# Optimization experiments

Measured on AMD Instinct MI355X. Metric: run time of the kernel, lower is better.

Reference implementation:

```python
import jax, jax.numpy as jnp
import numpy as np

NEG_SLOPE = 0.05

def leaky(x):
    return jnp.where(x >= 0, x, NEG_SLOPE * x)

def segment_softmax(e, seg, num_segments):
    m = jax.ops.segment_max(e, seg, num_segments=num_segments)
    ex = jnp.exp(e - m[seg])
    s = jax.ops.segment_sum(ex, seg, num_segments=num_segments)
    return ex / s[seg]

def scatter_mean(vals, seg, num_segments):
    tot = jax.ops.segment_sum(vals, seg, num_segments=num_segments)
    cnt = jax.ops.segment_sum(jnp.ones((vals.shape[0],), vals.dtype), seg, num_segments=num_segments)
    return tot / jnp.maximum(cnt, 1.0)[:, None]

def setup_inputs() -> dict:
    key = jax.random.key(0)
    ks = jax.random.split(key, 7)
    N, E, Fn, Fe, D = 50000, 800000, 128, 64, 64
    return {
        "x": jax.random.normal(ks[0], (N, Fn), jnp.float32),
        "edge_attr": jax.random.normal(ks[1], (E, Fe), jnp.float32),
        "edge_index": jax.random.randint(ks[2], (2, E), 0, N, jnp.int64),
        "W_node": jax.random.normal(ks[3], (D, Fn), jnp.float32) * 0.05,
        "W_edge": jax.random.normal(ks[4], (D, Fe), jnp.float32) * 0.05,
        "a_node": jax.random.normal(ks[5], (2 * D,), jnp.float32) * 0.05,
        "a_edge": jax.random.normal(ks[6], (2 * D,), jnp.float32) * 0.05,
    }

def reference(x, edge_attr, edge_index, W_node, W_edge, a_node, a_edge):
    N = x.shape[0]
    E = edge_index.shape[1]
    D = W_node.shape[0]
    h = x @ W_node.T           # [N, D]
    g = edge_attr @ W_edge.T   # [E, D]

    # ----- node->node branch (with self loops) -----
    loops = jnp.arange(N, dtype=edge_index.dtype)
    i_idx = jnp.concatenate([edge_index[0], loops])  # targets [E+N]
    j_idx = jnp.concatenate([edge_index[1], loops])  # sources [E+N]
    # attention score a^T [h_i || h_j] split into halves (no concat materialized)
    hi = h @ a_node[:D]   # [N]
    hj = h @ a_node[D:]   # [N]
    e_n = leaky(hi[i_idx] + hj[j_idx])               # [E+N]
    alpha_n = segment_softmax(e_n, i_idx, N)
    x_from_nodes = scatter_mean(alpha_n[:, None] * h[j_idx], i_idx, N)  # [N, D]

    # ----- edge->node branch (each edge attends from both endpoints) -----
    i_idx_e = jnp.concatenate([edge_index[0], edge_index[1]])           # [2E]
    g2 = jnp.concatenate([g, g], axis=0)                                # g[k_idx_e], [2E, D]
    he = h @ a_edge[:D]   # [N]
    ge = g @ a_edge[D:]   # [E]
    ge2 = jnp.concatenate([ge, ge])
    e_e = leaky(he[i_idx_e] + ge2)                                      # [2E]
    alpha_e = segment_softmax(e_e, i_idx_e, N)
    x_from_edges = scatter_mean(alpha_e[:, None] * g2, i_idx_e, N)      # [N, D]

    return jnp.concatenate([leaky(x_from_nodes), leaky(x_from_edges)], axis=-1)  # [N, 2D]
```

## Files before the change

kernel.cpp:

```cpp
#include <hip/hip_runtime.h>
#include <math.h>

#define NEG_SLOPE 0.05f

__device__ __forceinline__ float leaky(float x){ return x >= 0.f ? x : NEG_SLOPE * x; }

__device__ __forceinline__ unsigned short f2bf(float f){
    unsigned u = __float_as_uint(f);
    unsigned r = u + 0x7FFFu + ((u >> 16) & 1u);
    return (unsigned short)(r >> 16);
}
__device__ __forceinline__ float bf2f(unsigned short us){
    return __uint_as_float((unsigned)us << 16);
}

__global__ __launch_bounds__(256) void k_init(int* deg_n, int* deg_o, int* ctr, int N){
    int t = blockIdx.x * blockDim.x + threadIdx.x;
    if (t == 0){ ctr[0] = 0; ctr[1] = 0; }
    int stride = gridDim.x * blockDim.x;
    for (int i = t; i < N; i += stride){ deg_n[i] = 0; deg_o[i] = 0; }
}

template<int K, bool LEAKY, bool BF16OUT>
__global__ __launch_bounds__(256) void k_gemm64(const float* __restrict__ A, const float* __restrict__ B,
                                                float* __restrict__ C, unsigned short* __restrict__ Cb,
                                                int M, int ldC){
    __shared__ float As[K][68];
    __shared__ float Bs[K][68];
    const int m0 = blockIdx.x * 64;
    const int t = threadIdx.x;
    for (int i = t; i < 16 * K; i += 256){
        int d = i & 63, kq = i >> 6;
        float4 b = *(const float4*)&B[(size_t)d * K + kq * 4];
        Bs[kq*4+0][d] = b.x; Bs[kq*4+1][d] = b.y; Bs[kq*4+2][d] = b.z; Bs[kq*4+3][d] = b.w;
    }
    for (int i = t; i < 16 * K; i += 256){
        int r = i & 63, kq = i >> 6;
        int m = m0 + r;
        float4 a = make_float4(0.f, 0.f, 0.f, 0.f);
        if (m < M) a = *(const float4*)&A[(size_t)m * K + kq * 4];
        As[kq*4+0][r] = a.x; As[kq*4+1][r] = a.y; As[kq*4+2][r] = a.z; As[kq*4+3][r] = a.w;
    }
    __syncthreads();
    const int tx = t & 15, ty = t >> 4;
    float acc[4][4] = {};
    #pragma unroll 4
    for (int k = 0; k < K; k++){
        float4 a4 = *(const float4*)&As[k][ty * 4];
        float4 b4 = *(const float4*)&Bs[k][tx * 4];
        float av[4] = {a4.x, a4.y, a4.z, a4.w};
        float bv[4] = {b4.x, b4.y, b4.z, b4.w};
        #pragma unroll
        for (int r = 0; r < 4; r++)
            #pragma unroll
            for (int c = 0; c < 4; c++)
                acc[r][c] = fmaf(av[r], bv[c], acc[r][c]);
    }
    #pragma unroll
    for (int r = 0; r < 4; r++){
        int m = m0 + ty * 4 + r;
        if (m < M){
            float4 o;
            o.x = LEAKY ? leaky(acc[r][0]) : acc[r][0];
            o.y = LEAKY ? leaky(acc[r][1]) : acc[r][1];
            o.z = LEAKY ? leaky(acc[r][2]) : acc[r][2];
            o.w = LEAKY ? leaky(acc[r][3]) : acc[r][3];
            *(float4*)&C[(size_t)m * ldC + tx * 4] = o;
            if (BF16OUT){
                uint2 u;
                u.x = (unsigned)f2bf(o.x) | ((unsigned)f2bf(o.y) << 16);
                u.y = (unsigned)f2bf(o.z) | ((unsigned)f2bf(o.w) << 16);
                *(uint2*)&Cb[(size_t)m * 64 + tx * 4] = u;
            }
        }
    }
}

__global__ __launch_bounds__(256) void k_scal(const float* __restrict__ h,
        const float* __restrict__ a_node, const float* __restrict__ a_edge,
        float* __restrict__ hi, float* __restrict__ hj, float* __restrict__ he, int N){
    int i = blockIdx.x * 256 + threadIdx.x;
    if (i >= N) return;
    const float4* hr = (const float4*)(h + (size_t)i * 64);
    const float4* a1 = (const float4*)a_node;
    const float4* a2 = (const float4*)(a_node + 64);
    const float4* a3 = (const float4*)a_edge;
    float s1 = 0.f, s2 = 0.f, s3 = 0.f;
    #pragma unroll
    for (int q = 0; q < 16; q++){
        float4 v = hr[q], w1 = a1[q], w2 = a2[q], w3 = a3[q];
        s1 += v.x*w1.x + v.y*w1.y + v.z*w1.z + v.w*w1.w;
        s2 += v.x*w2.x + v.y*w2.y + v.z*w2.z + v.w*w2.w;
        s3 += v.x*w3.x + v.y*w3.y + v.z*w3.z + v.w*w3.w;
    }
    hi[i] = s1; hj[i] = s2; he[i] = s3;
}

__global__ __launch_bounds__(256) void k_ge(const float* __restrict__ ea,
        const float* __restrict__ We, const float* __restrict__ a_edge,
        float* __restrict__ ge, unsigned short* __restrict__ eab, int E){
    __shared__ float v[64];
    if (threadIdx.x < 64){
        float s = 0.f;
        for (int d = 0; d < 64; d++) s = fmaf(We[d * 64 + threadIdx.x], a_edge[64 + d], s);
        v[threadIdx.x] = s;
    }
    __syncthreads();
    int k = blockIdx.x * 256 + threadIdx.x;
    if (k >= E) return;
    const float4* row = (const float4*)(ea + (size_t)k * 64);
    uint2* brow = (uint2*)(eab + (size_t)k * 64);
    float s = 0.f;
    #pragma unroll
    for (int q = 0; q < 16; q++){
        float4 r = row[q];
        s = fmaf(r.x, v[4*q+0], s);
        s = fmaf(r.y, v[4*q+1], s);
        s = fmaf(r.z, v[4*q+2], s);
        s = fmaf(r.w, v[4*q+3], s);
        uint2 u;
        u.x = (unsigned)f2bf(r.x) | ((unsigned)f2bf(r.y) << 16);
        u.y = (unsigned)f2bf(r.z) | ((unsigned)f2bf(r.w) << 16);
        brow[q] = u;
    }
    ge[k] = s;
}

__global__ __launch_bounds__(256) void k_count(const int* __restrict__ idx,
        int* __restrict__ deg_n, int* __restrict__ deg_o, int E, int N){
    int g = blockIdx.x & 7;
    int lo = (int)(((long long)g * N) >> 3), hi = (int)(((long long)(g + 1) * N) >> 3);
    int nblk = gridDim.x >> 3;
    int start = ((blockIdx.x >> 3) * 256) + threadIdx.x;
    int stride = nblk * 256;
    for (int k = start; k < E; k += stride){
        int i0 = idx[k], i1 = idx[E + k];
        if (i0 >= lo && i0 < hi) atomicAdd(&deg_n[i0], 1);
        if (i1 >= lo && i1 < hi) atomicAdd(&deg_o[i1], 1);
    }
}

__global__ __launch_bounds__(256) void k_off(const int* __restrict__ deg_n, const int* __restrict__ deg_o,
        int* __restrict__ deg_e,
        int* __restrict__ off_n, int* __restrict__ cur_n,
        int* __restrict__ off_e, int* __restrict__ cur_e,
        int* __restrict__ ctr, int N){
    int i = blockIdx.x * 256 + threadIdx.x;
    int lane = threadIdx.x & 63;
    int dn = 0, de = 0;
    if (i < N){
        dn = deg_n[i];
        de = dn + deg_o[i];
    }
    int pn = dn, pe = de;
    #pragma unroll
    for (int d = 1; d < 64; d <<= 1){
        int on = __shfl_up(pn, d), oe = __shfl_up(pe, d);
        if (lane >= d){ pn += on; pe += oe; }
    }
    int base_n = 0, base_e = 0;
    if (lane == 63){
        base_n = atomicAdd(&ctr[0], pn);
        base_e = atomicAdd(&ctr[1], pe);
    }
    base_n = __shfl(base_n, 63);
    base_e = __shfl(base_e, 63);
    if (i < N){
        int on = base_n + pn - dn;
        int oe = base_e + pe - de;
        off_n[i] = on; cur_n[i] = on;
        off_e[i] = oe; cur_e[i] = oe;
        deg_e[i] = de;
    }
}

__global__ __launch_bounds__(256) void k_fill(const int* __restrict__ idx,
        const float* __restrict__ hj, const float* __restrict__ ge,
        int* __restrict__ cur_n, int* __restrict__ cur_e,
        int2* __restrict__ adj_n, int2* __restrict__ adj_e, int E, int N){
    int g = blockIdx.x & 7;
    int lo = (int)(((long long)g * N) >> 3), hi = (int)(((long long)(g + 1) * N) >> 3);
    int nblk = gridDim.x >> 3;
    int start = ((blockIdx.x >> 3) * 256) + threadIdx.x;
    int stride = nblk * 256;
    for (int k = start; k < E; k += stride){
        int i0 = idx[k], i1 = idx[E + k];
        bool t0 = (i0 >= lo && i0 < hi), t1 = (i1 >= lo && i1 < hi);
        if (t0 | t1){
            int gb = __float_as_int(ge[k]);
            if (t0){
                adj_n[atomicAdd(&cur_n[i0], 1)] = make_int2(i1, __float_as_int(hj[i1]));
                adj_e[atomicAdd(&cur_e[i0], 1)] = make_int2(k, gb);
            }
            if (t1) adj_e[atomicAdd(&cur_e[i1], 1)] = make_int2(k, gb);
        }
    }
}

__global__ __launch_bounds__(256) void k_out_n(const float* __restrict__ h,
        const unsigned short* __restrict__ hb,
        const float* __restrict__ hi, const float* __restrict__ hj,
        const int* __restrict__ off_n, const int* __restrict__ deg_n,
        const int2* __restrict__ adj_n,
        float* __restrict__ out, int N){
    int lane = threadIdx.x & 63;
    int i = (blockIdx.x * 256 + threadIdx.x) >> 6;
    if (i >= N) return;
    float hi_i = hi[i];
    float wself = __expf(leaky(hi_i + hj[i]));
    float s = wself;
    float acc = wself * h[(size_t)i * 64 + lane];
    int cnt = deg_n[i];
    int p = off_n[i], e = p + cnt;
    for (; p + 4 <= e; p += 4){
        int2 r0 = adj_n[p], r1 = adj_n[p+1], r2 = adj_n[p+2], r3 = adj_n[p+3];
        float v0 = bf2f(hb[(size_t)r0.x * 64 + lane]);
        float v1 = bf2f(hb[(size_t)r1.x * 64 + lane]);
        float v2 = bf2f(hb[(size_t)r2.x * 64 + lane]);
        float v3 = bf2f(hb[(size_t)r3.x * 64 + lane]);
        float w0 = __expf(leaky(hi_i + __int_as_float(r0.y)));
        float w1 = __expf(leaky(hi_i + __int_as_float(r1.y)));
        float w2 = __expf(leaky(hi_i + __int_as_float(r2.y)));
        float w3 = __expf(leaky(hi_i + __int_as_float(r3.y)));
        acc = fmaf(w0, v0, acc); acc = fmaf(w1, v1, acc);
        acc = fmaf(w2, v2, acc); acc = fmaf(w3, v3, acc);
        s += (w0 + w1) + (w2 + w3);
    }
    for (; p < e; p++){
        int2 r = adj_n[p];
        float v = bf2f(hb[(size_t)r.x * 64 + lane]);
        float w = __expf(leaky(hi_i + __int_as_float(r.y)));
        acc = fmaf(w, v, acc); s += w;
    }
    out[(size_t)i * 128 + lane] = leaky(acc / s / (float)(cnt + 1));
}

__global__ __launch_bounds__(256) void k_out_e(const unsigned short* __restrict__ eab,
        const float* __restrict__ he,
        const int* __restrict__ off_e, const int* __restrict__ deg_e,
        const int2* __restrict__ adj_e,
        float* __restrict__ acc_ea, int N){
    int lane = threadIdx.x & 63;
    int i = (blockIdx.x * 256 + threadIdx.x) >> 6;
    if (i >= N) return;
    float he_i = he[i];
    float s = 0.f, acc = 0.f;
    int cnt = deg_e[i];
    int p = off_e[i], e = p + cnt;
    for (; p + 4 <= e; p += 4){
        int2 r0 = adj_e[p], r1 = adj_e[p+1], r2 = adj_e[p+2], r3 = adj_e[p+3];
        float v0 = bf2f(eab[(size_t)r0.x * 64 + lane]);
        float v1 = bf2f(eab[(size_t)r1.x * 64 + lane]);
        float v2 = bf2f(eab[(size_t)r2.x * 64 + lane]);
        float v3 = bf2f(eab[(size_t)r3.x * 64 + lane]);
        float w0 = __expf(leaky(he_i + __int_as_float(r0.y)));
        float w1 = __expf(leaky(he_i + __int_as_float(r1.y)));
        float w2 = __expf(leaky(he_i + __int_as_float(r2.y)));
        float w3 = __expf(leaky(he_i + __int_as_float(r3.y)));
        acc = fmaf(w0, v0, acc); acc = fmaf(w1, v1, acc);
        acc = fmaf(w2, v2, acc); acc = fmaf(w3, v3, acc);
        s += (w0 + w1) + (w2 + w3);
    }
    for (; p < e; p++){
        int2 r = adj_e[p];
        float v = bf2f(eab[(size_t)r.x * 64 + lane]);
        float w = __expf(leaky(he_i + __int_as_float(r.y)));
        acc = fmaf(w, v, acc); s += w;
    }
    float val = (cnt > 0) ? (acc / s / (float)cnt) : 0.f;
    acc_ea[(size_t)i * 64 + lane] = val;
}

extern "C" void kernel_launch(void* const* d_in, const int* in_sizes, int n_in,
                              void* d_out, int out_size, void* d_ws, size_t ws_size,
                              hipStream_t stream){
    const float* x      = (const float*)d_in[0];
    const float* ea     = (const float*)d_in[1];
    const int*   idx    = (const int*)  d_in[2];
    const float* Wn     = (const float*)d_in[3];
    const float* We     = (const float*)d_in[4];
    const float* a_node = (const float*)d_in[5];
    const float* a_edge = (const float*)d_in[6];
    float* out = (float*)d_out;

    const int N = in_sizes[0] / 128;
    const int E = in_sizes[1] / 64;

    float* p = (float*)d_ws;
    float* h      = p; p += (size_t)N * 64;
    float* hi     = p; p += N;
    float* hj     = p; p += N;
    float* he     = p; p += N;
    float* ge     = p; p += E;
    float* acc_ea = p; p += (size_t)N * 64;
    unsigned short* hb  = (unsigned short*)p; p += (size_t)N * 32;
    unsigned short* eab = (unsigned short*)p; p += (size_t)E * 32;
    int* deg_n = (int*)p; p += N;
    int* deg_o = (int*)p; p += N;
    int* deg_e = (int*)p; p += N;
    int* off_n = (int*)p; p += N;
    int* off_e = (int*)p; p += N;
    int* cur_n = (int*)p; p += N;
    int* cur_e = (int*)p; p += N;
    int* ctr   = (int*)p; p += 2;
    int2* adj_n = (int2*)p; p += (size_t)2 * E;
    int2* adj_e = (int2*)p; p += (size_t)4 * E;

    k_init<<<256, 256, 0, stream>>>(deg_n, deg_o, ctr, N);
    k_gemm64<128, false, true><<<(N + 63) / 64, 256, 0, stream>>>(x, Wn, h, hb, N, 64);
    k_scal<<<(N + 255) / 256, 256, 0, stream>>>(h, a_node, a_edge, hi, hj, he, N);
    k_ge<<<(E + 255) / 256, 256, 0, stream>>>(ea, We, a_edge, ge, eab, E);
    k_count<<<1024, 256, 0, stream>>>(idx, deg_n, deg_o, E, N);
    k_off<<<(N + 255) / 256, 256, 0, stream>>>(deg_n, deg_o, deg_e, off_n, cur_n, off_e, cur_e, ctr, N);
    k_fill<<<1024, 256, 0, stream>>>(idx, hj, ge, cur_n, cur_e, adj_n, adj_e, E, N);
    k_out_n<<<(N + 3) / 4, 256, 0, stream>>>(h, hb, hi, hj, off_n, deg_n, adj_n, out, N);
    k_out_e<<<(N + 3) / 4, 256, 0, stream>>>(eab, he, off_e, deg_e, adj_e, acc_ea, N);
    k_gemm64<64, true, false><<<(N + 63) / 64, 256, 0, stream>>>(acc_ea, We, out + 64, nullptr, N, 128);
}
```

Baseline: 698.8 us.

## Fuse projection, degree counting and edge aggregation stages into fewer kernels

Folds the attention-scalar dot products into the node GEMM epilogue using wave shuffles. It merges the edge-attribute scoring and bf16 conversion with degree counting in a new row-coalesced k_ge2. The two aggregation kernels become one launch that splits blocks between the node and edge branches. The edge branch applies the W_edge projection in shared memory, so the acc_ea buffer and the final GEMM disappear. This cuts launches and global round trips of intermediates, but degree atomics are no longer partitioned by node range, which may hurt atomic locality.

```diff
diff --git a/kernel.cpp b/kernel.cpp
--- a/kernel.cpp
+++ b/kernel.cpp
@@ -14,17 +14,24 @@
     return __uint_as_float((unsigned)us << 16);
 }
 
-__global__ __launch_bounds__(256) void k_init(int* deg_n, int* deg_o, int* ctr, int N){
+__global__ __launch_bounds__(256) void k_init(int* deg_n, int* deg_o, int* ctr,
+        float* __restrict__ vv, const float* __restrict__ We, const float* __restrict__ a_edge, int N){
     int t = blockIdx.x * blockDim.x + threadIdx.x;
     if (t == 0){ ctr[0] = 0; ctr[1] = 0; }
+    if (t < 64){
+        float s = 0.f;
+        for (int d = 0; d < 64; d++) s = fmaf(We[d * 64 + t], a_edge[64 + d], s);
+        vv[t] = s;
+    }
     int stride = gridDim.x * blockDim.x;
     for (int i = t; i < N; i += stride){ deg_n[i] = 0; deg_o[i] = 0; }
 }
 
-template<int K, bool LEAKY, bool BF16OUT>
-__global__ __launch_bounds__(256) void k_gemm64(const float* __restrict__ A, const float* __restrict__ B,
-                                                float* __restrict__ C, unsigned short* __restrict__ Cb,
-                                                int M, int ldC){
+__global__ __launch_bounds__(256) void k_gemm_h(const float* __restrict__ A, const float* __restrict__ B,
+        const float* __restrict__ a_node, const float* __restrict__ a_edge,
+        float* __restrict__ C, unsigned short* __restrict__ Cb,
+        float* __restrict__ hi, float* __restrict__ hj, float* __restrict__ he, int M){
+    const int K = 128;
     __shared__ float As[K][68];
     __shared__ float Bs[K][68];
     const int m0 = blockIdx.x * 64;
@@ -60,83 +67,68 @@
     for (int r = 0; r < 4; r++){
         int m = m0 + ty * 4 + r;
         if (m < M){
-            float4 o;
-            o.x = LEAKY ? leaky(acc[r][0]) : acc[r][0];
-            o.y = LEAKY ? leaky(acc[r][1]) : acc[r][1];
-            o.z = LEAKY ? leaky(acc[r][2]) : acc[r][2];
-            o.w = LEAKY ? leaky(acc[r][3]) : acc[r][3];
-            *(float4*)&C[(size_t)m * ldC + tx * 4] = o;
-            if (BF16OUT){
-                uint2 u;
-                u.x = (unsigned)f2bf(o.x) | ((unsigned)f2bf(o.y) << 16);
-                u.y = (unsigned)f2bf(o.z) | ((unsigned)f2bf(o.w) << 16);
-                *(uint2*)&Cb[(size_t)m * 64 + tx * 4] = u;
-            }
-        }
-    }
-}
-
-__global__ __launch_bounds__(256) void k_scal(const float* __restrict__ h,
-        const float* __restrict__ a_node, const float* __restrict__ a_edge,
-        float* __restrict__ hi, float* __restrict__ hj, float* __restrict__ he, int N){
-    int i = blockIdx.x * 256 + threadIdx.x;
-    if (i >= N) return;
-    const float4* hr = (const float4*)(h + (size_t)i * 64);
-    const float4* a1 = (const float4*)a_node;
-    const float4* a2 = (const float4*)(a_node + 64);
-    const float4* a3 = (const float4*)a_edge;
-    float s1 = 0.f, s2 = 0.f, s3 = 0.f;
+            float4 o = make_float4(acc[r][0], acc[r][1], acc[r][2], acc[r][3]);
+            *(float4*)&C[(size_t)m * 64 + tx * 4] = o;
+            uint2 u;
+            u.x = (unsigned)f2bf(o.x) | ((unsigned)f2bf(o.y) << 16);
+            u.y = (unsigned)f2bf(o.z) | ((unsigned)f2bf(o.w) << 16);
+            *(uint2*)&Cb[(size_t)m * 64 + tx * 4] = u;
+        }
+    }
+    float4 an1 = *(const float4*)&a_node[tx * 4];
+    float4 an2 = *(const float4*)&a_node[64 + tx * 4];
+    float4 ae1 = *(const float4*)&a_edge[tx * 4];
+    float p1[4], p2[4], p3[4];
     #pragma unroll
-    for (int q = 0; q < 16; q++){
-        float4 v = hr[q], w1 = a1[q], w2 = a2[q], w3 = a3[q];
-        s1 += v.x*w1.x + v.y*w1.y + v.z*w1.z + v.w*w1.w;
-        s2 += v.x*w2.x + v.y*w2.y + v.z*w2.z + v.w*w2.w;
-        s3 += v.x*w3.x + v.y*w3.y + v.z*w3.z + v.w*w3.w;
-    }
-    hi[i] = s1; hj[i] = s2; he[i] = s3;
-}
-
-__global__ __launch_bounds__(256) void k_ge(const float* __restrict__ ea,
-        const float* __restrict__ We, const float* __restrict__ a_edge,
-        float* __restrict__ ge, unsigned short* __restrict__ eab, int E){
-    __shared__ float v[64];
-    if (threadIdx.x < 64){
-        float s = 0.f;
-        for (int d = 0; d < 64; d++) s = fmaf(We[d * 64 + threadIdx.x], a_edge[64 + d], s);
-        v[threadIdx.x] = s;
-    }
-    __syncthreads();
-    int k = blockIdx.x * 256 + threadIdx.x;
-    if (k >= E) return;
-    const float4* row = (const float4*)(ea + (size_t)k * 64);
-    uint2* brow = (uint2*)(eab + (size_t)k * 64);
-    float s = 0.f;
+    for (int r = 0; r < 4; r++){
+        p1[r] = acc[r][0]*an1.x + acc[r][1]*an1.y + acc[r][2]*an1.z + acc[r][3]*an1.w;
+        p2[r] = acc[r][0]*an2.x + acc[r][1]*an2.y + acc[r][2]*an2.z + acc[r][3]*an2.w;
+        p3[r] = acc[r][0]*ae1.x + acc[r][1]*ae1.y + acc[r][2]*ae1.z + acc[r][3]*ae1.w;
+    }
     #pragma unroll
-    for (int q = 0; q < 16; q++){
-        float4 r = row[q];
-        s = fmaf(r.x, v[4*q+0], s);
-        s = fmaf(r.y, v[4*q+1], s);
-        s = fmaf(r.z, v[4*q+2], s);
-        s = fmaf(r.w, v[4*q+3], s);
-        uint2 u;
-        u.x = (unsigned)f2bf(r.x) | ((unsigned)f2bf(r.y) << 16);
-        u.y = (unsigned)f2bf(r.z) | ((unsigned)f2bf(r.w) << 16);
-        brow[q] = u;
-    }
-    ge[k] = s;
-}
-
-__global__ __launch_bounds__(256) void k_count(const int* __restrict__ idx,
-        int* __restrict__ deg_n, int* __restrict__ deg_o, int E, int N){
-    int g = blockIdx.x & 7;
-    int lo = (int)(((long long)g * N) >> 3), hi = (int)(((long long)(g + 1) * N) >> 3);
-    int nblk = gridDim.x >> 3;
-    int start = ((blockIdx.x >> 3) * 256) + threadIdx.x;
-    int stride = nblk * 256;
-    for (int k = start; k < E; k += stride){
-        int i0 = idx[k], i1 = idx[E + k];
-        if (i0 >= lo && i0 < hi) atomicAdd(&deg_n[i0], 1);
-        if (i1 >= lo && i1 < hi) atomicAdd(&deg_o[i1], 1);
+    for (int m = 1; m < 16; m <<= 1){
+        #pragma unroll
+        for (int r = 0; r < 4; r++){
+            p1[r] += __shfl_xor(p1[r], m);
+            p2[r] += __shfl_xor(p2[r], m);
+            p3[r] += __shfl_xor(p3[r], m);
+        }
+    }
+    if (tx == 0){
+        #pragma unroll
+        for (int r = 0; r < 4; r++){
+            int m = m0 + ty * 4 + r;
+            if (m < M){ hi[m] = p1[r]; hj[m] = p2[r]; he[m] = p3[r]; }
+        }
+    }
+}
+
+__global__ __launch_bounds__(256) void k_ge2(const float* __restrict__ ea, const int* __restrict__ idx,
+        const float* __restrict__ vv, float* __restrict__ ge, unsigned short* __restrict__ eab,
+        int* __restrict__ deg_n, int* __restrict__ deg_o, int E){
+    int l = threadIdx.x & 63;
+    int gw = (blockIdx.x * 256 + threadIdx.x) >> 6;
+    int nw = (gridDim.x * 256) >> 6;
+    int seg = l & 15, rl = l >> 4;
+    float4 v4 = *(const float4*)&vv[seg * 4];
+    for (int r0 = gw * 4; r0 < E; r0 += nw * 4){
+        int row = r0 + rl;
+        if (row < E){
+            float4 a = *(const float4*)&ea[(size_t)row * 64 + seg * 4];
+            float s = a.x*v4.x + a.y*v4.y + a.z*v4.z + a.w*v4.w;
+            uint2 u;
+            u.x = (unsigned)f2bf(a.x) | ((unsigned)f2bf(a.y) << 16);
+            u.y = (unsigned)f2bf(a.z) | ((unsigned)f2bf(a.w) << 16);
+            *(uint2*)&eab[(size_t)row * 64 + seg * 4] = u;
+            #pragma unroll
+            for (int m = 1; m < 16; m <<= 1) s += __shfl_xor(s, m);
+            if (seg == 0){
+                ge[row] = s;
+                int i0 = idx[row], i1 = idx[E + row];
+                atomicAdd(&deg_n[i0], 1);
+                atomicAdd(&deg_o[i1], 1);
+            }
+        }
     }
 }
 
@@ -197,78 +189,100 @@
     }
 }
 
-__global__ __launch_bounds__(256) void k_out_n(const float* __restrict__ h,
-        const unsigned short* __restrict__ hb,
-        const float* __restrict__ hi, const float* __restrict__ hj,
-        const int* __restrict__ off_n, const int* __restrict__ deg_n,
-        const int2* __restrict__ adj_n,
-        float* __restrict__ out, int N){
+__global__ __launch_bounds__(256) void k_out(const float* __restrict__ h,
+        const unsigned short* __restrict__ hb, const unsigned short* __restrict__ eab,
+        const float* __restrict__ hi, const float* __restrict__ hj, const float* __restrict__ he,
+        const float* __restrict__ We,
+        const int* __restrict__ off_n, const int* __restrict__ deg_n, const int2* __restrict__ adj_n,
+        const int* __restrict__ off_e, const int* __restrict__ deg_e, const int2* __restrict__ adj_e,
+        float* __restrict__ out, int N, int nb_node){
+    __shared__ float WeT[64][65];
+    __shared__ float valS[4][64];
     int lane = threadIdx.x & 63;
-    int i = (blockIdx.x * 256 + threadIdx.x) >> 6;
-    if (i >= N) return;
-    float hi_i = hi[i];
-    float wself = __expf(leaky(hi_i + hj[i]));
-    float s = wself;
-    float acc = wself * h[(size_t)i * 64 + lane];
-    int cnt = deg_n[i];
-    int p = off_n[i], e = p + cnt;
-    for (; p + 4 <= e; p += 4){
-        int2 r0 = adj_n[p], r1 = adj_n[p+1], r2 = adj_n[p+2], r3 = adj_n[p+3];
-        float v0 = bf2f(hb[(size_t)r0.x * 64 + lane]);
-        float v1 = bf2f(hb[(size_t)r1.x * 64 + lane]);
-        float v2 = bf2f(hb[(size_t)r2.x * 64 + lane]);
-        float v3 = bf2f(hb[(size_t)r3.x * 64 + lane]);
-        float w0 = __expf(leaky(hi_i + __int_as_float(r0.y)));
-        float w1 = __expf(leaky(hi_i + __int_as_float(r1.y)));
-        float w2 = __expf(leaky(hi_i + __int_as_float(r2.y)));
-        float w3 = __expf(leaky(hi_i + __int_as_float(r3.y)));
-        acc = fmaf(w0, v0, acc); acc = fmaf(w1, v1, acc);
-        acc = fmaf(w2, v2, acc); acc = fmaf(w3, v3, acc);
-        s += (w0 + w1) + (w2 + w3);
-    }
-    for (; p < e; p++){
-        int2 r = adj_n[p];
-        float v = bf2f(hb[(size_t)r.x * 64 + lane]);
-        float w = __expf(leaky(hi_i + __int_as_float(r.y)));
-        acc = fmaf(w, v, acc); s += w;
-    }
-    out[(size_t)i * 128 + lane] = leaky(acc / s / (float)(cnt + 1));
-}
-
-__global__ __launch_bounds__(256) void k_out_e(const unsigned short* __restrict__ eab,
-        const float* __restrict__ he,
-        const int* __restrict__ off_e, const int* __restrict__ deg_e,
-        const int2* __restrict__ adj_e,
-        float* __restrict__ acc_ea, int N){
-    int lane = threadIdx.x & 63;
-    int i = (blockIdx.x * 256 + threadIdx.x) >> 6;
-    if (i >= N) return;
-    float he_i = he[i];
-    float s = 0.f, acc = 0.f;
-    int cnt = deg_e[i];
-    int p = off_e[i], e = p + cnt;
-    for (; p + 4 <= e; p += 4){
-        int2 r0 = adj_e[p], r1 = adj_e[p+1], r2 = adj_e[p+2], r3 = adj_e[p+3];
-        float v0 = bf2f(eab[(size_t)r0.x * 64 + lane]);
-        float v1 = bf2f(eab[(size_t)r1.x * 64 + lane]);
-        float v2 = bf2f(eab[(size_t)r2.x * 64 + lane]);
-        float v3 = bf2f(eab[(size_t)r3.x * 64 + lane]);
-        float w0 = __expf(leaky(he_i + __int_as_float(r0.y)));
-        float w1 = __expf(leaky(he_i + __int_as_float(r1.y)));
-        float w2 = __expf(leaky(he_i + __int_as_float(r2.y)));
-        float w3 = __expf(leaky(he_i + __int_as_float(r3.y)));
-        acc = fmaf(w0, v0, acc); acc = fmaf(w1, v1, acc);
-        acc = fmaf(w2, v2, acc); acc = fmaf(w3, v3, acc);
-        s += (w0 + w1) + (w2 + w3);
-    }
-    for (; p < e; p++){
-        int2 r = adj_e[p];
-        float v = bf2f(eab[(size_t)r.x * 64 + lane]);
-        float w = __expf(leaky(he_i + __int_as_float(r.y)));
-        acc = fmaf(w, v, acc); s += w;
-    }
-    float val = (cnt > 0) ? (acc / s / (float)cnt) : 0.f;
-    acc_ea[(size_t)i * 64 + lane] = val;
+    int w = threadIdx.x >> 6;
+
+    if (blockIdx.x < nb_node){
+        int i = (blockIdx.x * 256 + (int)threadIdx.x) >> 6;
+        if (i >= N) return;
+        float hi_i = hi[i];
+        float wself = __expf(leaky(hi_i + hj[i]));
+        float s = wself;
+        float acc = wself * h[(size_t)i * 64 + lane];
+        int cnt = deg_n[i];
+        int p = off_n[i], e = p + cnt;
+        for (; p + 4 <= e; p += 4){
+            int2 r0 = adj_n[p], r1 = adj_n[p+1], r2 = adj_n[p+2], r3 = adj_n[p+3];
+            float v0 = bf2f(hb[(size_t)r0.x * 64 + lane]);
+            float v1 = bf2f(hb[(size_t)r1.x * 64 + lane]);
+            float v2 = bf2f(hb[(size_t)r2.x * 64 + lane]);
+            float v3 = bf2f(hb[(size_t)r3.x * 64 + lane]);
+            float w0 = __expf(leaky(hi_i + __int_as_float(r0.y)));
+            float w1 = __expf(leaky(hi_i + __int_as_float(r1.y)));
+            float w2 = __expf(leaky(hi_i + __int_as_float(r2.y)));
+            float w3 = __expf(leaky(hi_i + __int_as_float(r3.y)));
+            acc = fmaf(w0, v0, acc); acc = fmaf(w1, v1, acc);
+            acc = fmaf(w2, v2, acc); acc = fmaf(w3, v3, acc);
+            s += (w0 + w1) + (w2 + w3);
+        }
+        for (; p < e; p++){
+            int2 r = adj_n[p];
+            float v = bf2f(hb[(size_t)r.x * 64 + lane]);
+            float wgt = __expf(leaky(hi_i + __int_as_float(r.y)));
+            acc = fmaf(wgt, v, acc); s += wgt;
+        }
+        out[(size_t)i * 128 + lane] = leaky(acc / s / (float)(cnt + 1));
+    } else {
+        for (int t2 = threadIdx.x; t2 < 1024; t2 += 256){
+            int d = t2 >> 4, c0 = (t2 & 15) * 4;
+            float4 v = *(const float4*)&We[d * 64 + c0];
+            WeT[c0+0][d] = v.x; WeT[c0+1][d] = v.y; WeT[c0+2][d] = v.z; WeT[c0+3][d] = v.w;
+        }
+        int i = ((blockIdx.x - nb_node) * 256 + (int)threadIdx.x) >> 6;
+        float val = 0.f;
+        int iok = (i < N);
+        if (iok){
+            float he_i = he[i];
+            float s = 0.f, acc = 0.f;
+            int cnt = deg_e[i];
+            int p = off_e[i], e = p + cnt;
+            for (; p + 4 <= e; p += 4){
+                int2 r0 = adj_e[p], r1 = adj_e[p+1], r2 = adj_e[p+2], r3 = adj_e[p+3];
+                float v0 = bf2f(eab[(size_t)r0.x * 64 + lane]);
+                float v1 = bf2f(eab[(size_t)r1.x * 64 + lane]);
+                float v2 = bf2f(eab[(size_t)r2.x * 64 + lane]);
+                float v3 = bf2f(eab[(size_t)r3.x * 64 + lane]);
+                float w0 = __expf(leaky(he_i + __int_as_float(r0.y)));
+                float w1 = __expf(leaky(he_i + __int_as_float(r1.y)));
+                float w2 = __expf(leaky(he_i + __int_as_float(r2.y)));
+                float w3 = __expf(leaky(he_i + __int_as_float(r3.y)));
+                acc = fmaf(w0, v0, acc); acc = fmaf(w1, v1, acc);
+                acc = fmaf(w2, v2, acc); acc = fmaf(w3, v3, acc);
+                s += (w0 + w1) + (w2 + w3);
+            }
+            for (; p < e; p++){
+                int2 r = adj_e[p];
+                float v = bf2f(eab[(size_t)r.x * 64 + lane]);
+                float wgt = __expf(leaky(he_i + __int_as_float(r.y)));
+                acc = fmaf(wgt, v, acc); s += wgt;
+            }
+            val = (cnt > 0) ? (acc / s / (float)cnt) : 0.f;
+        }
+        __syncthreads();
+        valS[w][lane] = val;
+        __syncthreads();
+        if (iok){
+            float acc2 = 0.f;
+            #pragma unroll
+            for (int c4 = 0; c4 < 16; c4++){
+                float4 vb = *(const float4*)&valS[w][c4 * 4];
+                acc2 = fmaf(vb.x, WeT[c4*4+0][lane], acc2);
+                acc2 = fmaf(vb.y, WeT[c4*4+1][lane], acc2);
+                acc2 = fmaf(vb.z, WeT[c4*4+2][lane], acc2);
+                acc2 = fmaf(vb.w, WeT[c4*4+3][lane], acc2);
+            }
+            out[(size_t)i * 128 + 64 + lane] = leaky(acc2);
+        }
+    }
 }
 
 extern "C" void kernel_launch(void* const* d_in, const int* in_sizes, int n_in,
@@ -292,7 +306,7 @@
     float* hj     = p; p += N;
     float* he     = p; p += N;
     float* ge     = p; p += E;
-    float* acc_ea = p; p += (size_t)N * 64;
+    float* vv     = p; p += 64;
     unsigned short* hb  = (unsigned short*)p; p += (size_t)N * 32;
     unsigned short* eab = (unsigned short*)p; p += (size_t)E * 32;
     int* deg_n = (int*)p; p += N;
@@ -302,18 +316,17 @@
     int* off_e = (int*)p; p += N;
     int* cur_n = (int*)p; p += N;
     int* cur_e = (int*)p; p += N;
-    int* ctr   = (int*)p; p += 2;
+    int* ctr   = (int*)p; p += 4;
     int2* adj_n = (int2*)p; p += (size_t)2 * E;
     int2* adj_e = (int2*)p; p += (size_t)4 * E;
 
-    k_init<<<256, 256, 0, stream>>>(deg_n, deg_o, ctr, N);
-    k_gemm64<128, false, true><<<(N + 63) / 64, 256, 0, stream>>>(x, Wn, h, hb, N, 64);
-    k_scal<<<(N + 255) / 256, 256, 0, stream>>>(h, a_node, a_edge, hi, hj, he, N);
-    k_ge<<<(E + 255) / 256, 256, 0, stream>>>(ea, We, a_edge, ge, eab, E);
-    k_count<<<1024, 256, 0, stream>>>(idx, deg_n, deg_o, E, N);
+    const int nb = (N + 3) / 4;
+
+    k_init<<<256, 256, 0, stream>>>(deg_n, deg_o, ctr, vv, We, a_edge, N);
+    k_gemm_h<<<(N + 63) / 64, 256, 0, stream>>>(x, Wn, a_node, a_edge, h, hb, hi, hj, he, N);
+    k_ge2<<<2048, 256, 0, stream>>>(ea, idx, vv, ge, eab, deg_n, deg_o, E);
     k_off<<<(N + 255) / 256, 256, 0, stream>>>(deg_n, deg_o, deg_e, off_n, cur_n, off_e, cur_e, ctr, N);
     k_fill<<<1024, 256, 0, stream>>>(idx, hj, ge, cur_n, cur_e, adj_n, adj_e, E, N);
-    k_out_n<<<(N + 3) / 4, 256, 0, stream>>>(h, hb, hi, hj, off_n, deg_n, adj_n, out, N);
-    k_out_e<<<(N + 3) / 4, 256, 0, stream>>>(eab, he, off_e, deg_e, adj_e, acc_ea, N);
-    k_gemm64<64, true, false><<<(N + 63) / 64, 256, 0, stream>>>(acc_ea, We, out + 64, nullptr, N, 128);
-}
+    k_out<<<2 * nb, 256, 0, stream>>>(h, hb, eab, hi, hj, he, We,
+                                      off_n, deg_n, adj_n, off_e, deg_e, adj_e, out, N, nb);
+}
```

New measurement: 611.8 us. 12.5% less time.
